# Kernel tuning notes

Hardware: AMD Instinct MI355X
Metric: run time of the kernel (lower is better)

## Reference

```python
import jax, jax.numpy as jnp
import numpy as np

B, T, O = 8, 8, 25
C, H, W = 3, 192, 640
P = 16            # pooled output size / patch size
D = 768           # embed dim
GH, GW = 12, 2    # max adaptive sampling grid: ceil(H/P), ceil(2*r_max/P)


def setup_inputs() -> dict:
    key = jax.random.key(0)
    k1, k2, k3, k4, k5, k6 = jax.random.split(key, 6)
    features = jax.random.normal(k1, (B, C, T, H, W), jnp.float32)
    # keypoints (x, y, r); x >= H so that the source's buggy y2=min(x+r,H) still yields valid boxes
    kx = jax.random.uniform(k2, (B, T, O), minval=float(H), maxval=float(W))
    ky = jax.random.uniform(k3, (B, T, O), minval=0.0, maxval=float(H))
    kr = jax.random.uniform(k4, (B, T, O), minval=4.0, maxval=16.0)
    keypoints = jnp.stack([kx, ky, kr], axis=-1)
    conv_w = jax.random.normal(k5, (D, C, P, P), jnp.float32) * (1.0 / np.sqrt(C * P * P))
    conv_b = jax.random.normal(k6, (D,), jnp.float32) * 0.01
    return {"features": features, "keypoints": keypoints, "conv_w": conv_w, "conv_b": conv_b}


def _sample_coords(start, bin_sz, grid, G, size):
    # start,bin_sz,grid: [N]; returns coords y/x [N,P,G], validity mask, low idx, high idx, lerp weight
    N = start.shape[0]
    pb = jnp.arange(P, dtype=start.dtype)
    ig = jnp.arange(G, dtype=start.dtype)
    gf = jnp.maximum(grid, 1).astype(start.dtype)
    c = (start[:, None, None]
         + pb[None, :, None] * bin_sz[:, None, None]
         + (ig[None, None, :] + 0.5) * (bin_sz / gf)[:, None, None])  # [N,P,G]
    valid = (jnp.arange(G)[None, None, :] < grid[:, None, None]) & (c >= -1.0) & (c <= float(size))
    cc = jnp.clip(c, 0.0, float(size - 1))
    lo = jnp.floor(cc).astype(jnp.int32)
    hi = jnp.minimum(lo + 1, size - 1)
    l = cc - lo.astype(cc.dtype)  # fractional part (ly/lx)
    return valid, lo, hi, l


def _roi_align(feats_hw, boxes, img_idx):
    # feats_hw: [BT,H,W,C]; boxes: [N,4] xyxy; torchvision roi_align, aligned=True, sampling_ratio=-1
    x1, y1, x2, y2 = boxes[:, 0], boxes[:, 1], boxes[:, 2], boxes[:, 3]
    start_h, start_w = y1 - 0.5, x1 - 0.5  # aligned offset (spatial_scale=1)
    roi_h, roi_w = y2 - y1, x2 - x1        # aligned=True: no clamp to >=1
    bin_h, bin_w = roi_h / P, roi_w / P
    gh = jnp.ceil(roi_h / P).astype(jnp.int32)
    gw = jnp.ceil(roi_w / P).astype(jnp.int32)
    count = jnp.maximum(gh * gw, 1).astype(feats_hw.dtype)

    vy, y0, y1i, ly = _sample_coords(start_h, bin_h, gh, GH, H)  # [N,P,GH]
    vx, x0, x1i, lx = _sample_coords(start_w, bin_w, gw, GW, W)  # [N,P,GW]
    hy, hx = 1.0 - ly, 1.0 - lx

    def gather(yi, xi):  # -> [N,Ph,Pw,GH,GW,C]
        return feats_hw[img_idx[:, None, None, None, None],
                        yi[:, :, None, :, None],
                        xi[:, None, :, None, :]]

    w00 = hy[:, :, None, :, None] * hx[:, None, :, None, :]
    w01 = hy[:, :, None, :, None] * lx[:, None, :, None, :]
    w10 = ly[:, :, None, :, None] * hx[:, None, :, None, :]
    w11 = ly[:, :, None, :, None] * lx[:, None, :, None, :]
    val = (w00[..., None] * gather(y0, x0) + w01[..., None] * gather(y0, x1i)
           + w10[..., None] * gather(y1i, x0) + w11[..., None] * gather(y1i, x1i))
    mask = (vy[:, :, None, :, None] & vx[:, None, :, None, :])[..., None]
    val = jnp.where(mask, val, 0.0)
    return val.sum(axis=(3, 4)) / count[:, None, None, None]  # [N,P,P,C]


def _forward(features, keypoints, conv_w, conv_b):
    feats_hw = features.transpose(0, 2, 3, 4, 1).reshape(B * T, H, W, C)  # (b t) h w c
    kpts = keypoints.reshape(B * T * O, 3)
    kx, ky, kr = kpts[:, 0], kpts[:, 1], kpts[:, 2]
    # faithful to source (note: y2 uses x, a bug in the original module)
    bx1 = jnp.maximum(kx - kr, 0.0)
    by1 = jnp.maximum(ky - kr, 0.0)
    bx2 = jnp.minimum(kx + kr, float(W))
    by2 = jnp.minimum(kx + kr, float(H))
    boxes = jnp.stack([bx1, by1, bx2, by2], axis=-1)
    img_idx = jnp.arange(B * T * O, dtype=jnp.int32) // O
    pooled = _roi_align(feats_hw, boxes, img_idx)  # [N,P,P,C]
    # PxP conv with no padding on PxP input == flatten + linear
    out = jnp.einsum('nijc,dcij->nd', pooled, conv_w) + conv_b
    return out.reshape(B, T, O, D)


def reference(features, keypoints, conv_w, conv_b):
    return _forward(features, keypoints, conv_w, conv_b)
```

## Files before the change

kernel.cpp:

```cpp
#include <hip/hip_runtime.h>

#define NB 8
#define NT 8
#define NO 25
#define NC 3
#define NH 192
#define NW 640
#define NP 16
#define ND 768
#define NGH 12
#define NGW 2
#define NKP (NB*NT*NO)
#define NK (NC*NP*NP)
#define NTASK (NKP*NC)
#define NSPLIT (NTASK*2)
#define NCVW ((NK*ND)/(256*4))

#define S_STRIDE 42
#define S_ROWS 100

typedef __attribute__((ext_vector_type(4))) float  f32x4;
typedef __attribute__((ext_vector_type(8))) short  bf16x8;

static __device__ __forceinline__ unsigned short f2bf(float f) {
  union { float f; unsigned u; } x; x.f = f;
  unsigned r = x.u + 0x7FFFu + ((x.u >> 16) & 1u);
  return (unsigned short)(r >> 16);
}

__global__ __launch_bounds__(256) void pool_convw_kernel(
    const float* __restrict__ features,
    const float* __restrict__ keypoints,
    const float* __restrict__ conv_w,
    unsigned short* __restrict__ pooled,
    unsigned short* __restrict__ wbf)
{
  __shared__ float S[S_ROWS * S_STRIDE + 16];

  const int bid = blockIdx.x;
  const int tid = threadIdx.x;

  if (bid < NCVW) {
    const int i = bid * 256 + tid;
    const float4 v = reinterpret_cast<const float4*>(conv_w)[i];
    ushort4 o;
    o.x = f2bf(v.x); o.y = f2bf(v.y); o.z = f2bf(v.z); o.w = f2bf(v.w);
    reinterpret_cast<ushort4*>(wbf)[i] = o;
    return;
  }

  const int rb      = bid - NCVW;
  const int logical = (rb & 7) * (NSPLIT / 8) + (rb >> 3);
  const int task    = logical >> 1;
  const int half    = logical & 1;
  const int n  = task / 3;
  const int ch = task - 3 * n;

  const float kx = keypoints[n * 3 + 0];
  const float ky = keypoints[n * 3 + 1];
  const float kr = keypoints[n * 3 + 2];

  const float bx1 = fmaxf(kx - kr, 0.0f);
  const float by1 = fmaxf(ky - kr, 0.0f);
  const float bx2 = fminf(kx + kr, (float)NW);
  const float by2 = fminf(kx + kr, (float)NH);

  const float start_h = by1 - 0.5f;
  const float start_w = bx1 - 0.5f;
  const float bin_h = (by2 - by1) * (1.0f / (float)NP);
  const float bin_w = (bx2 - bx1) * (1.0f / (float)NP);
  const int gh = (int)ceilf(bin_h);
  const int gw = (int)ceilf(bin_w);
  const float ghf = (float)max(gh, 1);
  const float gwf = (float)max(gw, 1);
  const float inv_count = 1.0f / (float)max(gh * gw, 1);
  const float sub_h = bin_h / ghf;
  const float sub_w = bin_w / gwf;

  const int i_lo = half << 3;

  const float cy_min = start_h + (float)i_lo * bin_h + 0.5f * sub_h;
  const float cy_max = start_h + (float)(i_lo + 7) * bin_h + ((float)(gh - 1) + 0.5f) * sub_h;
  const float cx_min = start_w + 0.5f * sub_w;
  const float cx_max = start_w + 15.0f * bin_w + ((float)(gw - 1) + 0.5f) * sub_w;
  const int rmin = (int)floorf(fminf(fmaxf(cy_min, 0.0f), (float)(NH - 1)));
  const int rmax = min((int)floorf(fminf(fmaxf(cy_max, 0.0f), (float)(NH - 1))) + 1, NH - 1);
  const int cmin = (int)floorf(fminf(fmaxf(cx_min, 0.0f), (float)(NW - 1)));
  const int cmax = min((int)floorf(fminf(fmaxf(cx_max, 0.0f), (float)(NW - 1))) + 1, NW - 1);
  const int nrows = rmax - rmin + 1;
  const int cmin_al = cmin & ~3;
  const int nq = ((cmax - cmin_al) >> 2) + 1;
  const int tot = nrows * nq;
  const float inv_nq = 1.0f / (float)nq;

  const int img  = n / NO;
  const int bb   = img / NT;
  const int timg = img - bb * NT;
  const float* __restrict__ src =
      features + (size_t)((bb * NC + ch) * NT + timg) * (NH * NW);

  float4 v0, v1, v2, v3;
  int ro0, ro1, ro2, ro3;

#define STAGE_LOAD(Q, V, RO)                                                 \
  {                                                                          \
    const int e = tid + (Q << 8);                                            \
    if (e < tot) {                                                           \
      const int r  = (int)(((float)e + 0.5f) * inv_nq);                      \
      const int c4 = (e - r * nq) << 2;                                      \
      const int gc = cmin_al + c4;                                           \
      const float* p = src + (size_t)(rmin + r) * NW + gc;                   \
      if (gc + 3 < NW) { V = *reinterpret_cast<const float4*>(p); }          \
      else { V.x = p[0]; V.y = p[min(1, NW - 1 - gc)];                       \
             V.z = p[min(2, NW - 1 - gc)]; V.w = p[min(3, NW - 1 - gc)]; }   \
      RO = r * S_STRIDE + c4;                                                \
    } else { RO = -1; }                                                      \
  }

  STAGE_LOAD(0, v0, ro0) STAGE_LOAD(1, v1, ro1)
  STAGE_LOAD(2, v2, ro2) STAGE_LOAD(3, v3, ro3)
#undef STAGE_LOAD

#define STAGE_WRITE(V, RO)                                                   \
  if (RO >= 0) { float* s = &S[RO];                                          \
    s[0] = V.x; s[1] = V.y; s[2] = V.z; s[3] = V.w; }

  STAGE_WRITE(v0, ro0) STAGE_WRITE(v1, ro1)
  STAGE_WRITE(v2, ro2) STAGE_WRITE(v3, ro3)
#undef STAGE_WRITE

  if (tid < nrows) {
    float* pz = &S[tid * S_STRIDE + (nq << 2)];
    pz[0] = 0.0f; pz[1] = 0.0f;
  }

  __syncthreads();

  const int i = i_lo + (tid >> 5);
  const int j = (tid >> 1) & 15;
  const int h = tid & 1;

  const float c0x = fminf(fmaxf(start_w + (float)j * bin_w + 0.5f * sub_w, 0.0f), (float)(NW - 1));
  const float c1x = fminf(fmaxf(start_w + (float)j * bin_w + 1.5f * sub_w, 0.0f), (float)(NW - 1));
  const int x00 = (int)floorf(c0x);
  const int x01 = (int)floorf(c1x);
  const float lx0 = c0x - (float)x00;
  const float hx0 = 1.0f - lx0;
  const float w1f = (gw > 1) ? 1.0f : 0.0f;
  const float lx1 = w1f * (c1x - (float)x01);
  const float hx1 = w1f * (1.0f - (c1x - (float)x01));
  const int xbg = x00 & ~1;
  const int xb  = xbg - cmin_al;
  const int d0  = x00 - xbg;
  const int d1  = x01 - xbg;

  const float xw0 = (d0 == 0 ? hx0 : 0.0f) + (d1 == 0 ? hx1 : 0.0f);
  const float xw1 = (d0 == 1 ? hx0 : 0.0f) + (d0 == 0 ? lx0 : 0.0f)
                  + (d1 == 1 ? hx1 : 0.0f) + (d1 == 0 ? lx1 : 0.0f);
  const float xw2 = (d0 == 1 ? lx0 : 0.0f)
                  + (d1 == 2 ? hx1 : 0.0f) + (d1 == 1 ? lx1 : 0.0f);
  const float xw3 = (d1 == 2 ? lx1 : 0.0f);

  float acc = 0.0f;
#pragma unroll
  for (int gg = 0; gg < 6; ++gg) {
    const int gy = h * 6 + gg;
    const float c = start_h + (float)i * bin_h + ((float)gy + 0.5f) * sub_h;
    const float cc = fminf(fmaxf(c, 0.0f), (float)(NH - 1));
    const int y0 = (int)floorf(cc);
    const float ly = cc - (float)y0;
    const bool vy = gy < gh;
    const float wl = vy ? ly : 0.0f;
    const float wh = vy ? 1.0f - ly : 0.0f;
    const int r0  = min(y0 - rmin, nrows - 1);
    const int ry0 = r0 * S_STRIDE + xb;
    const int ry1 = min(r0 + 1, nrows - 1) * S_STRIDE + xb;
    const float2* p0 = reinterpret_cast<const float2*>(&S[ry0]);
    const float2* p1 = reinterpret_cast<const float2*>(&S[ry1]);
    const float2 t0 = p0[0], t1 = p0[1];
    const float2 b0 = p1[0], b1 = p1[1];
    const float dotT = xw0 * t0.x + xw1 * t0.y + xw2 * t1.x + xw3 * t1.y;
    const float dotB = xw0 * b0.x + xw1 * b0.y + xw2 * b1.x + xw3 * b1.y;
    acc += wh * dotT + wl * dotB;
  }
  acc += __shfl_xor(acc, 1);
  if (h == 0)
    pooled[(size_t)n * NK + ch * (NP * NP) + (i << 4) + j] = f2bf(acc * inv_count);
}

#define BM 64
#define BN 64
#define BK 64

static __device__ __forceinline__ void gld_lds16(const unsigned short* g,
                                                 unsigned short* l) {
  __builtin_amdgcn_global_load_lds(
      (const __attribute__((address_space(1))) unsigned int*)g,
      (__attribute__((address_space(3))) unsigned int*)l,
      16, 0, 0);
}

__global__ __launch_bounds__(256) void gemm_kernel(
    const unsigned short* __restrict__ A,
    const unsigned short* __restrict__ Bw,
    const float* __restrict__ bias,
    float* __restrict__ outp)
{
  __shared__ __align__(16) unsigned short As[2][BM * BK];
  __shared__ __align__(16) unsigned short Bs[2][BM * BK];

  const int tid = threadIdx.x;
  const int w = tid >> 6;
  const int l = tid & 63;
  const int bm = blockIdx.x * BM;
  const int bn = blockIdx.y * BN;

  const int wr = w >> 1, wc = w & 1;
  const int lr = l & 15;
  const int kh = l >> 4;

  const int rA0 = (wr << 5) + lr;
  const int rB0 = (wc << 5) + lr;

#define STAGE(buf, kk)                                                       \
  {                                                                          \
    _Pragma("unroll")                                                        \
    for (int q = 0; q < 2; ++q) {                                            \
      const int s   = (q << 8) + tid;                                        \
      const int row = s >> 3;                                                \
      const int c16 = (s & 7) ^ (row & 7);                                   \
      gld_lds16(A  + (size_t)(bm + row) * NK + (kk) + (c16 << 3),            \
                &As[buf][s << 3]);                                           \
      gld_lds16(Bw + (size_t)(bn + row) * NK + (kk) + (c16 << 3),            \
                &Bs[buf][s << 3]);                                           \
    }                                                                        \
  }

  f32x4 acc[2][2] = {};

  STAGE(0, 0)
  __syncthreads();

  int cur = 0;
  for (int it = 0; it < NK / BK; ++it) {
    if (it + 1 < NK / BK) STAGE(cur ^ 1, (it + 1) * BK)

#pragma unroll
    for (int ks = 0; ks < 2; ++ks) {
      const int kq = (ks << 2) + kh;
      const bf16x8 a0 = *reinterpret_cast<const bf16x8*>(
          &As[cur][(rA0 << 6) + ((kq ^ (rA0 & 7)) << 3)]);
      const bf16x8 a1 = *reinterpret_cast<const bf16x8*>(
          &As[cur][((rA0 + 16) << 6) + ((kq ^ ((rA0 + 16) & 7)) << 3)]);
      const bf16x8 b0 = *reinterpret_cast<const bf16x8*>(
          &Bs[cur][(rB0 << 6) + ((kq ^ (rB0 & 7)) << 3)]);
      const bf16x8 b1 = *reinterpret_cast<const bf16x8*>(
          &Bs[cur][((rB0 + 16) << 6) + ((kq ^ ((rB0 + 16) & 7)) << 3)]);
      acc[0][0] = __builtin_amdgcn_mfma_f32_16x16x32_bf16(a0, b0, acc[0][0], 0, 0, 0);
      acc[0][1] = __builtin_amdgcn_mfma_f32_16x16x32_bf16(a0, b1, acc[0][1], 0, 0, 0);
      acc[1][0] = __builtin_amdgcn_mfma_f32_16x16x32_bf16(a1, b0, acc[1][0], 0, 0, 0);
      acc[1][1] = __builtin_amdgcn_mfma_f32_16x16x32_bf16(a1, b1, acc[1][1], 0, 0, 0);
    }

    __syncthreads();
    cur ^= 1;
  }
#undef STAGE

#pragma unroll
  for (int ni = 0; ni < 2; ++ni) {
    const int col = bn + (wc << 5) + (ni << 4) + lr;
    const float bv = bias[col];
#pragma unroll
    for (int mi = 0; mi < 2; ++mi) {
      const int rbase = bm + (wr << 5) + (mi << 4) + (kh << 2);
#pragma unroll
      for (int q = 0; q < 4; ++q) {
        outp[(size_t)(rbase + q) * ND + col] = acc[mi][ni][q] + bv;
      }
    }
  }
}

extern "C" void kernel_launch(void* const* d_in, const int* in_sizes, int n_in,
                              void* d_out, int out_size, void* d_ws, size_t ws_size,
                              hipStream_t stream) {
  (void)in_sizes; (void)n_in; (void)out_size; (void)ws_size;
  const float* features  = (const float*)d_in[0];
  const float* keypoints = (const float*)d_in[1];
  const float* conv_w    = (const float*)d_in[2];
  const float* conv_b    = (const float*)d_in[3];
  float* outp = (float*)d_out;

  unsigned short* pooled = (unsigned short*)d_ws;
  unsigned short* wbf    = (unsigned short*)((char*)d_ws + 2457600);

  pool_convw_kernel<<<NCVW + NSPLIT, 256, 0, stream>>>(features, keypoints,
                                                       conv_w, pooled, wbf);

  dim3 grid(NKP / BM, ND / BN);
  gemm_kernel<<<grid, 256, 0, stream>>>(pooled, wbf, conv_b, outp);
}
```

Baseline: 38.31 us.

## Pool all three channels per block, sharing ROI geometry and address math

Each pooling block now handles every channel of one keypoint-half instead of a single channel. The ROI geometry, staging addresses and bilinear weights are computed once and reused across three LDS slabs, which cuts the block count by three and issues twelve independent global loads per thread. In exchange LDS use per block triples, which may reduce occupancy. The GEMM LDS swizzle for the +16 rows is simplified to reuse the rA0&7 term, which is equivalent since 16 mod 8 is 0. The edge-column load now clamps to NW-4 instead of doing scalar loads, which shifts staged data when the window reaches the image edge.

New measurement: 37.94 us. About the same (-1.0%).

```diff
diff --git a/kernel.cpp b/kernel.cpp
--- a/kernel.cpp
+++ b/kernel.cpp
@@ -12,12 +12,12 @@
 #define NGW 2
 #define NKP (NB*NT*NO)
 #define NK (NC*NP*NP)
-#define NTASK (NKP*NC)
-#define NSPLIT (NTASK*2)
+#define NHALF (NKP*2)
 #define NCVW ((NK*ND)/(256*4))
 
 #define S_STRIDE 42
 #define S_ROWS 100
+#define S_SLAB (S_ROWS * S_STRIDE)
 
 typedef __attribute__((ext_vector_type(4))) float  f32x4;
 typedef __attribute__((ext_vector_type(8))) short  bf16x8;
@@ -35,7 +35,7 @@
     unsigned short* __restrict__ pooled,
     unsigned short* __restrict__ wbf)
 {
-  __shared__ float S[S_ROWS * S_STRIDE + 16];
+  __shared__ float S[3 * S_SLAB + 16];
 
   const int bid = blockIdx.x;
   const int tid = threadIdx.x;
@@ -50,11 +50,9 @@
   }
 
   const int rb      = bid - NCVW;
-  const int logical = (rb & 7) * (NSPLIT / 8) + (rb >> 3);
-  const int task    = logical >> 1;
+  const int logical = (rb & 7) * (NHALF / 8) + (rb >> 3);
+  const int n       = logical >> 1;
   const int half    = logical & 1;
-  const int n  = task / 3;
-  const int ch = task - 3 * n;
 
   const float kx = keypoints[n * 3 + 0];
   const float ky = keypoints[n * 3 + 1];
@@ -96,42 +94,50 @@
   const int img  = n / NO;
   const int bb   = img / NT;
   const int timg = img - bb * NT;
-  const float* __restrict__ src =
-      features + (size_t)((bb * NC + ch) * NT + timg) * (NH * NW);
-
-  float4 v0, v1, v2, v3;
+  const float* __restrict__ src0 =
+      features + (size_t)((bb * NC + 0) * NT + timg) * (NH * NW);
+  const size_t chs = (size_t)NT * NH * NW;
+
+  float4 a0, a1, a2, a3, b0, b1, b2, b3, c0, c1, c2, c3;
   int ro0, ro1, ro2, ro3;
-
-#define STAGE_LOAD(Q, V, RO)                                                 \
+  int go0, go1, go2, go3;
+
+#define ADDR(Q, RO, GO)                                                      \
   {                                                                          \
     const int e = tid + (Q << 8);                                            \
     if (e < tot) {                                                           \
       const int r  = (int)(((float)e + 0.5f) * inv_nq);                      \
       const int c4 = (e - r * nq) << 2;                                      \
-      const int gc = cmin_al + c4;                                           \
-      const float* p = src + (size_t)(rmin + r) * NW + gc;                   \
-      if (gc + 3 < NW) { V = *reinterpret_cast<const float4*>(p); }          \
-      else { V.x = p[0]; V.y = p[min(1, NW - 1 - gc)];                       \
-             V.z = p[min(2, NW - 1 - gc)]; V.w = p[min(3, NW - 1 - gc)]; }   \
+      int gc = cmin_al + c4;                                                 \
+      if (gc + 3 >= NW) gc = NW - 4;      \
+      GO = (rmin + r) * NW + gc;                                             \
       RO = r * S_STRIDE + c4;                                                \
-    } else { RO = -1; }                                                      \
-  }
-
-  STAGE_LOAD(0, v0, ro0) STAGE_LOAD(1, v1, ro1)
-  STAGE_LOAD(2, v2, ro2) STAGE_LOAD(3, v3, ro3)
-#undef STAGE_LOAD
-
-#define STAGE_WRITE(V, RO)                                                   \
-  if (RO >= 0) { float* s = &S[RO];                                          \
+    } else { RO = -1; GO = 0; }                                              \
+  }
+  ADDR(0, ro0, go0) ADDR(1, ro1, go1) ADDR(2, ro2, go2) ADDR(3, ro3, go3)
+#undef ADDR
+
+
+#define LD(V, GO, RO, CH)                                                    \
+  if (RO >= 0) V = *reinterpret_cast<const float4*>(src0 + chs * CH + GO);
+  LD(a0, go0, ro0, 0) LD(a1, go1, ro1, 0) LD(a2, go2, ro2, 0) LD(a3, go3, ro3, 0)
+  LD(b0, go0, ro0, 1) LD(b1, go1, ro1, 1) LD(b2, go2, ro2, 1) LD(b3, go3, ro3, 1)
+  LD(c0, go0, ro0, 2) LD(c1, go1, ro1, 2) LD(c2, go2, ro2, 2) LD(c3, go3, ro3, 2)
+#undef LD
+
+#define ST(V, RO, CH)                                                        \
+  if (RO >= 0) { float* s = &S[CH * S_SLAB + RO];                            \
     s[0] = V.x; s[1] = V.y; s[2] = V.z; s[3] = V.w; }
-
-  STAGE_WRITE(v0, ro0) STAGE_WRITE(v1, ro1)
-  STAGE_WRITE(v2, ro2) STAGE_WRITE(v3, ro3)
-#undef STAGE_WRITE
+  ST(a0, ro0, 0) ST(a1, ro1, 0) ST(a2, ro2, 0) ST(a3, ro3, 0)
+  ST(b0, ro0, 1) ST(b1, ro1, 1) ST(b2, ro2, 1) ST(b3, ro3, 1)
+  ST(c0, ro0, 2) ST(c1, ro1, 2) ST(c2, ro2, 2) ST(c3, ro3, 2)
+#undef ST
 
   if (tid < nrows) {
-    float* pz = &S[tid * S_STRIDE + (nq << 2)];
-    pz[0] = 0.0f; pz[1] = 0.0f;
+    const int o = tid * S_STRIDE + (nq << 2);
+    S[o] = 0.0f; S[o + 1] = 0.0f;
+    S[S_SLAB + o] = 0.0f; S[S_SLAB + o + 1] = 0.0f;
+    S[2 * S_SLAB + o] = 0.0f; S[2 * S_SLAB + o + 1] = 0.0f;
   }
 
   __syncthreads();
@@ -161,7 +167,7 @@
                   + (d1 == 2 ? hx1 : 0.0f) + (d1 == 1 ? lx1 : 0.0f);
   const float xw3 = (d1 == 2 ? lx1 : 0.0f);
 
-  float acc = 0.0f;
+  float acc0 = 0.0f, acc1 = 0.0f, acc2 = 0.0f;
 #pragma unroll
   for (int gg = 0; gg < 6; ++gg) {
     const int gy = h * 6 + gg;
@@ -175,17 +181,27 @@
     const int r0  = min(y0 - rmin, nrows - 1);
     const int ry0 = r0 * S_STRIDE + xb;
     const int ry1 = min(r0 + 1, nrows - 1) * S_STRIDE + xb;
-    const float2* p0 = reinterpret_cast<const float2*>(&S[ry0]);
-    const float2* p1 = reinterpret_cast<const float2*>(&S[ry1]);
-    const float2 t0 = p0[0], t1 = p0[1];
-    const float2 b0 = p1[0], b1 = p1[1];
-    const float dotT = xw0 * t0.x + xw1 * t0.y + xw2 * t1.x + xw3 * t1.y;
-    const float dotB = xw0 * b0.x + xw1 * b0.y + xw2 * b1.x + xw3 * b1.y;
-    acc += wh * dotT + wl * dotB;
-  }
-  acc += __shfl_xor(acc, 1);
-  if (h == 0)
-    pooled[(size_t)n * NK + ch * (NP * NP) + (i << 4) + j] = f2bf(acc * inv_count);
+#pragma unroll
+    for (int ch = 0; ch < 3; ++ch) {
+      const float2* p0 = reinterpret_cast<const float2*>(&S[ch * S_SLAB + ry0]);
+      const float2* p1 = reinterpret_cast<const float2*>(&S[ch * S_SLAB + ry1]);
+      const float2 t0 = p0[0], t1 = p0[1];
+      const float2 u0 = p1[0], u1 = p1[1];
+      const float dotT = xw0 * t0.x + xw1 * t0.y + xw2 * t1.x + xw3 * t1.y;
+      const float dotB = xw0 * u0.x + xw1 * u0.y + xw2 * u1.x + xw3 * u1.y;
+      const float d = wh * dotT + wl * dotB;
+      if (ch == 0) acc0 += d; else if (ch == 1) acc1 += d; else acc2 += d;
+    }
+  }
+  acc0 += __shfl_xor(acc0, 1);
+  acc1 += __shfl_xor(acc1, 1);
+  acc2 += __shfl_xor(acc2, 1);
+  if (h == 0) {
+    const size_t base = (size_t)n * NK + (i << 4) + j;
+    pooled[base]           = f2bf(acc0 * inv_count);
+    pooled[base + NP * NP]     = f2bf(acc1 * inv_count);
+    pooled[base + 2 * NP * NP] = f2bf(acc2 * inv_count);
+  }
 }
 
 #define BM 64
@@ -251,11 +267,11 @@
       const bf16x8 a0 = *reinterpret_cast<const bf16x8*>(
           &As[cur][(rA0 << 6) + ((kq ^ (rA0 & 7)) << 3)]);
       const bf16x8 a1 = *reinterpret_cast<const bf16x8*>(
-          &As[cur][((rA0 + 16) << 6) + ((kq ^ ((rA0 + 16) & 7)) << 3)]);
+          &As[cur][((rA0 + 16) << 6) + ((kq ^ (rA0 & 7)) << 3)]);
       const bf16x8 b0 = *reinterpret_cast<const bf16x8*>(
           &Bs[cur][(rB0 << 6) + ((kq ^ (rB0 & 7)) << 3)]);
       const bf16x8 b1 = *reinterpret_cast<const bf16x8*>(
-          &Bs[cur][((rB0 + 16) << 6) + ((kq ^ ((rB0 + 16) & 7)) << 3)]);
+          &Bs[cur][((rB0 + 16) << 6) + ((kq ^ (rB0 & 7)) << 3)]);
       acc[0][0] = __builtin_amdgcn_mfma_f32_16x16x32_bf16(a0, b0, acc[0][0], 0, 0, 0);
       acc[0][1] = __builtin_amdgcn_mfma_f32_16x16x32_bf16(a0, b1, acc[0][1], 0, 0, 0);
       acc[1][0] = __builtin_amdgcn_mfma_f32_16x16x32_bf16(a1, b0, acc[1][0], 0, 0, 0);
@@ -295,8 +311,8 @@
   unsigned short* pooled = (unsigned short*)d_ws;
   unsigned short* wbf    = (unsigned short*)((char*)d_ws + 2457600);
 
-  pool_convw_kernel<<<NCVW + NSPLIT, 256, 0, stream>>>(features, keypoints,
-                                                       conv_w, pooled, wbf);
+  pool_convw_kernel<<<NCVW + NHALF, 256, 0, stream>>>(features, keypoints,
+                                                      conv_w, pooled, wbf);
 
   dim3 grid(NKP / BM, ND / BN);
   gemm_kernel<<<grid, 256, 0, stream>>>(pooled, wbf, conv_b, outp);
```
